# Performance work log

Hardware: AMD Instinct MI355X
Metric: run time of the kernel (lower is better)

Reference implementation:

```python
import math
import jax, jax.numpy as jnp
import numpy as np

B, L, HID = 2, 2048, 2048
H = 16
D = HID // H  # 128
EPS = 1e-6
ROPE_BASE = 10000.0
BETA_MIN, BETA_MAX = 0.8, 0.9995


def _rope_cache(seq_len, dim):
    half = dim // 2
    inv_freq = 1.0 / (ROPE_BASE ** (jnp.arange(half, dtype=jnp.float32) / float(half)))
    t = jnp.arange(seq_len, dtype=jnp.float32)
    freqs = t[:, None] * inv_freq[None, :]  # [L, half]
    return jnp.cos(freqs), jnp.sin(freqs)


def _apply_rope(x, cos, sin):
    # x: [B, H, L, D]; cos/sin: [L, D//2]
    half = x.shape[-1] // 2
    xe, xo = x[..., :half], x[..., half:]
    c = cos[None, None]
    s = sin[None, None]
    return jnp.concatenate([xe * c - xo * s, xe * s + xo * c], axis=-1)


def setup_inputs() -> dict:
    key = jax.random.key(0)
    ks = jax.random.split(key, 6)
    sc = 1.0 / math.sqrt(HID)  # ~ xavier scale
    return {
        "x": jax.random.normal(ks[0], (B, L, HID), jnp.float32),
        "Wq": jax.random.normal(ks[1], (HID, HID), jnp.float32) * sc,
        "Wk": jax.random.normal(ks[2], (HID, HID), jnp.float32) * sc,
        "Wv": jax.random.normal(ks[3], (HID, HID), jnp.float32) * sc,
        "Wg": jax.random.normal(ks[4], (HID, H), jnp.float32) * sc,
        "bg": jnp.full((H,), math.log(0.98 / (1.0 - 0.98)), jnp.float32),
        "Wo": jax.random.normal(ks[5], (HID, HID), jnp.float32) * sc,
        "bo": jnp.zeros((HID,), jnp.float32),
    }


def _deltanet(x, Wq, Wk, Wv, Wg, bg, Wo, bo):
    Bb, Ll, _ = x.shape
    split = lambda t: t.reshape(Bb, Ll, H, D).transpose(0, 2, 1, 3)  # [B,H,L,D]
    q = split(x @ Wq)
    k = split(x @ Wk)
    v = split(x @ Wv)

    cos, sin = _rope_cache(Ll, D)
    q = _apply_rope(q, cos, sin)
    k = _apply_rope(k, cos, sin)

    beta = jax.nn.sigmoid(x @ Wg + bg)                # [B,L,H]
    beta = jnp.clip(beta, BETA_MIN, BETA_MAX).transpose(0, 2, 1)  # [B,H,L]

    phi_q = jax.nn.elu(q) + 1.0
    phi_k = jax.nn.elu(k) + 1.0

    # time-major for scan
    pq = phi_q.transpose(2, 0, 1, 3)  # [L,B,H,D]
    pk = phi_k.transpose(2, 0, 1, 3)
    vt = v.transpose(2, 0, 1, 3)
    bt = beta.transpose(2, 0, 1)      # [L,B,H]

    S0 = jnp.zeros((Bb, H, D, D), jnp.float32)
    z0 = jnp.zeros((Bb, H, D), jnp.float32)

    def step(carry, inp):
        S, z = carry
        pq_t, pk_t, v_t, b_t = inp
        S = S * b_t[..., None, None] + pk_t[..., :, None] * v_t[..., None, :]
        z = z * b_t[..., None] + pk_t
        numer = jnp.einsum('bhd,bhde->bhe', pq_t, S)
        denom = jnp.sum(pq_t * z, axis=-1, keepdims=True) + EPS
        return (S, z), numer / denom

    (_, _), y = jax.lax.scan(step, (S0, z0), (pq, pk, vt, bt))  # y: [L,B,H,D]
    y = y.transpose(1, 0, 2, 3).reshape(Bb, Ll, HID)  # [B,L,H*D]
    return y @ Wo + bo


def reference(x, Wq, Wk, Wv, Wg, bg, Wo, bo):
    return _deltanet(x, Wq, Wk, Wv, Wg, bg, Wo, bo)
```

## Files before the change

### kernel.cpp

```cpp
#include <hip/hip_runtime.h>


typedef __attribute__((ext_vector_type(8))) short short8;
typedef __attribute__((ext_vector_type(4))) float f32x4;

__device__ __forceinline__ unsigned short f2bf(float f) {
  unsigned u = __float_as_uint(f);
  u += 0x7fffu + ((u >> 16) & 1u);
  return (unsigned short)(u >> 16);
}
__device__ __forceinline__ float bf2f(unsigned short s) {
  return __uint_as_float(((unsigned)s) << 16);
}
__device__ __forceinline__ float phi_elu1(float x) {
  return x > 0.f ? x + 1.f : expf(x);
}
__device__ __forceinline__ void gl_lds16(const void* g, void* l) {
  __builtin_amdgcn_global_load_lds(
      (const __attribute__((address_space(1))) void*)g,
      (__attribute__((address_space(3))) void*)l, 16, 0, 0);
}
__device__ __forceinline__ void bar_raw() {
  asm volatile("" ::: "memory");
  __builtin_amdgcn_s_barrier();
  asm volatile("" ::: "memory");
}

__global__ __launch_bounds__(256)
void k_cast(const float* __restrict__ x, unsigned short* __restrict__ xb) {
  int i = (blockIdx.x * 256 + threadIdx.x) * 4;
  float4 f = *(const float4*)(x + i);
  uint2 p;
  p.x = (unsigned)f2bf(f.x) | ((unsigned)f2bf(f.y) << 16);
  p.y = (unsigned)f2bf(f.z) | ((unsigned)f2bf(f.w) << 16);
  *(uint2*)(xb + i) = p;
}

__global__ __launch_bounds__(256)
void k_transw(const float* __restrict__ Wq, const float* __restrict__ Wk,
              const float* __restrict__ Wv, const float* __restrict__ Wo,
              const float* __restrict__ Wg,
              unsigned short* __restrict__ Wt, unsigned short* __restrict__ Wot,
              unsigned short* __restrict__ Wgt16) {
  const int z = blockIdx.z;
  if (z == 4) {
    if (blockIdx.y != 0) return;
    int idx = blockIdx.x * 256 + threadIdx.x;
    int h = idx >> 9, k4 = (idx & 511) * 4;
    uint2 p;
    p.x = (unsigned)f2bf(Wg[(k4 + 0) * 16 + h]) | ((unsigned)f2bf(Wg[(k4 + 1) * 16 + h]) << 16);
    p.y = (unsigned)f2bf(Wg[(k4 + 2) * 16 + h]) | ((unsigned)f2bf(Wg[(k4 + 3) * 16 + h]) << 16);
    *(uint2*)(Wgt16 + (size_t)h * 2048 + k4) = p;
    return;
  }
  const float* W = (z == 0) ? Wq : (z == 1) ? Wk : (z == 2) ? Wv : Wo;
  unsigned short* out = (z < 3) ? (Wt + (size_t)z * 2048 * 2048) : Wot;
  __shared__ float tile[64][65];
  const int n0 = blockIdx.x * 64;
  const int k0 = blockIdx.y * 64;
  const int tx = threadIdx.x & 63;
  const int ty = threadIdx.x >> 6;
#pragma unroll
  for (int rl = 0; rl < 16; ++rl) {
    int kk = rl * 4 + ty;
    tile[kk][tx] = W[(size_t)(k0 + kk) * 2048 + n0 + tx];
  }
  __syncthreads();
#pragma unroll
  for (int rl = 0; rl < 16; ++rl) {
    int nn = rl * 4 + ty;
    out[(size_t)(n0 + nn) * 2048 + k0 + tx] = f2bf(tile[tx][nn]);
  }
}

__global__ __launch_bounds__(256)
void k_betaW(const unsigned short* __restrict__ xb, const unsigned short* __restrict__ Wgt16,
             const float* __restrict__ bg, float* __restrict__ beta) {
  const int w = threadIdx.x >> 6;
  const int lane = threadIdx.x & 63;
  const int m = blockIdx.x * 4 + w;
  const int h = lane & 15, kq = lane >> 4;
  const unsigned short* xr = xb + (size_t)m * 2048 + kq * 512;
  const unsigned short* wr = Wgt16 + (size_t)h * 2048 + kq * 512;
  float acc = 0.f;
#pragma unroll 8
  for (int i = 0; i < 64; ++i) {
    short8 xv = *(const short8*)(xr + i * 8);
    short8 wv = *(const short8*)(wr + i * 8);
#pragma unroll
    for (int j = 0; j < 8; ++j)
      acc = fmaf(bf2f((unsigned short)xv[j]), bf2f((unsigned short)wv[j]), acc);
  }
  acc += __shfl_xor(acc, 16, 64);
  acc += __shfl_xor(acc, 32, 64);
  if (lane < 16) {
    float v = acc + bg[h];
    float bv = 1.f / (1.f + expf(-v));
    beta[(size_t)m * 16 + h] = fminf(fmaxf(bv, 0.8f), 0.9995f);
  }
}

template <bool OUT_BF16, bool ADD_BIAS>
__global__ __launch_bounds__(512, 2)
void k_gemm2(const unsigned short* __restrict__ A, const unsigned short* __restrict__ Bt,
             void* __restrict__ Cptr, const float* __restrict__ bias,
             int M, int N, int K, int ldA, int ldC) {
  __shared__ __align__(16) unsigned short Ls[3][3][128][64];
  const int tid = threadIdx.x;
  const int lane = tid & 63;
  const int w = tid >> 6;
  const int wm = w >> 1;
  const int wn = w & 1;
  const int ql = lane >> 4;
  const int r = lane & 15;

  const int nwg = gridDim.x * gridDim.y;
  const int orig = blockIdx.y * gridDim.x + blockIdx.x;
  const int li = (orig & 7) * (nwg >> 3) + (orig >> 3);
  const int m0 = (li & 15) * 256;
  const int n0 = (li >> 4) * 128;

  const int srow = tid >> 3;
  const int sphys = tid & 7;
  const int slog = sphys ^ (srow & 7);
  const unsigned short* Ab = A + (size_t)(m0 + srow) * ldA + slog * 8;
  const unsigned short* Bb = Bt + (size_t)(n0 + srow) * K + slog * 8;

#define STG(st, h, tt)                                                        \
  do {                                                                        \
    const size_t ldx = ((h) == 2) ? (size_t)K : (size_t)ldA;                  \
    const unsigned short* gs =                                                \
        (((h) == 2) ? Bb : (Ab + (size_t)((h) * 128) * ldA)) +                \
        (size_t)(tt) * 64;                                                    \
    unsigned short* ld = &Ls[(st)][(h)][srow][sphys * 8];                     \
    gl_lds16(gs, ld);                                                         \
    gl_lds16(gs + 64 * ldx, ld + 64 * 64);                                    \
  } while (0)

  f32x4 acc[4][4];
#pragma unroll
  for (int i = 0; i < 4; ++i)
#pragma unroll
    for (int j = 0; j < 4; ++j) acc[i][j] = (f32x4){0.f, 0.f, 0.f, 0.f};

  const int NT = K >> 6;

#pragma unroll
  for (int h = 0; h < 3; ++h) STG(0, h, 0);
#pragma unroll
  for (int h = 0; h < 3; ++h) STG(1, h, 1);
  asm volatile("s_waitcnt vmcnt(6)" ::: "memory");
  bar_raw();

  short8 bfr[4][2];

  for (int t = 0; t < NT; ++t) {
    const int st = t % 3;
    const unsigned short (*LA)[64] = Ls[st][wm >> 1];
    const unsigned short (*LB)[64] = Ls[st][2];
    const int arow0 = (wm & 1) * 64;
    const int brow0 = wn * 64;
    const bool pf = (t + 2 < NT);
    const int s2 = (t + 2) % 3;
#pragma unroll
    for (int p = 0; p < 2; ++p) {
      if (p == 0) {
#pragma unroll
        for (int nj = 0; nj < 4; ++nj)
#pragma unroll
          for (int kk = 0; kk < 2; ++kk)
            bfr[nj][kk] = *(const short8*)
                &LB[brow0 + nj * 16 + r][((kk * 4 + ql) ^ (r & 7)) * 8];
      }
      short8 af[2][2];
#pragma unroll
      for (int im = 0; im < 2; ++im)
#pragma unroll
        for (int kk = 0; kk < 2; ++kk)
          af[im][kk] = *(const short8*)
              &LA[arow0 + (p * 2 + im) * 16 + r][((kk * 4 + ql) ^ (r & 7)) * 8];
      if (pf) {
        if (p == 0) {
          STG(s2, 0, t + 2);
          STG(s2, 1, t + 2);
        } else {
          STG(s2, 2, t + 2);
        }
      }
      bar_raw();
      asm volatile("s_waitcnt lgkmcnt(0)" ::: "memory");
      __builtin_amdgcn_sched_barrier(0);
      __builtin_amdgcn_s_setprio(1);
#pragma unroll
      for (int kk = 0; kk < 2; ++kk)
#pragma unroll
        for (int im = 0; im < 2; ++im)
#pragma unroll
          for (int nj = 0; nj < 4; ++nj)
            acc[p * 2 + im][nj] = __builtin_amdgcn_mfma_f32_16x16x32_bf16(
                af[im][kk], bfr[nj][kk], acc[p * 2 + im][nj], 0, 0, 0);
      __builtin_amdgcn_s_setprio(0);
      if (p == 1) {
        if (pf)
          asm volatile("s_waitcnt vmcnt(6)" ::: "memory");
        else if (t + 1 < NT)
          asm volatile("s_waitcnt vmcnt(0)" ::: "memory");
      }
      bar_raw();
    }
  }
#undef STG

#pragma unroll
  for (int mi = 0; mi < 4; ++mi) {
#pragma unroll
    for (int nj = 0; nj < 4; ++nj) {
#pragma unroll
      for (int rr = 0; rr < 4; ++rr) {
        int mrow = m0 + wm * 64 + mi * 16 + ql * 4 + rr;
        int ncol = n0 + wn * 64 + nj * 16 + r;
        float val = acc[mi][nj][rr];
        if (ADD_BIAS) val += bias[ncol];
        if (OUT_BF16)
          ((unsigned short*)Cptr)[(size_t)mrow * ldC + ncol] = f2bf(val);
        else
          ((float*)Cptr)[(size_t)mrow * ldC + ncol] = val;
      }
    }
  }
}

__global__ __launch_bounds__(256)
void k_prep(const unsigned short* __restrict__ qkv, const float* __restrict__ beta,
            unsigned short* __restrict__ Qt, unsigned short* __restrict__ Ktg,
            unsigned short* __restrict__ Ag, float* __restrict__ gch) {
  const int ch = blockIdx.x;
  const int bh = blockIdx.y;
  const int b = bh >> 4, h = bh & 15;
  const int tid = threadIdx.x;
  const int t0 = ch * 64;

  __shared__ float Gs[64];
  __shared__ unsigned short Qs[64][136];
  __shared__ unsigned short Ks[64][136];

  if (tid < 64) {
    float bb = beta[((size_t)(b * 2048 + t0 + tid)) * 16 + h];
#pragma unroll
    for (int off = 1; off < 64; off <<= 1) {
      float o = __shfl_up(bb, off, 64);
      if (tid >= off) bb *= o;
    }
    Gs[tid] = bb;
    if (tid == 63) gch[bh * 32 + ch] = bb;
  }
  __syncthreads();

  const int dgl = tid & 7;
  float invf[8];
#pragma unroll
  for (int j = 0; j < 8; ++j)
    invf[j] = expf((float)(dgl * 8 + j) * -0.14391156831212787f);

  int s = tid >> 3;
#pragma unroll
  for (int rep = 0; rep < 2; ++rep, s += 32) {
    size_t row = ((size_t)(b * 2048 + t0 + s)) * 6144 + (size_t)h * 128;
    short8 qlo = *(const short8*)(qkv + row + dgl * 8);
    short8 qhi = *(const short8*)(qkv + row + 64 + dgl * 8);
    short8 klo = *(const short8*)(qkv + row + 2048 + dgl * 8);
    short8 khi = *(const short8*)(qkv + row + 2048 + 64 + dgl * 8);
    float g = Gs[s];
    float ig = 1.f / g;
    float tg = (float)(t0 + s);
    short8 oql, oqh, okl, okh;
#pragma unroll
    for (int j = 0; j < 8; ++j) {
      float sn, cs;
      __sincosf(tg * invf[j], &sn, &cs);
      float qe = bf2f((unsigned short)qlo[j]), qo = bf2f((unsigned short)qhi[j]);
      float a0 = qe * cs - qo * sn, a1 = qe * sn + qo * cs;
      oql[j] = (short)f2bf(phi_elu1(a0) * g);
      oqh[j] = (short)f2bf(phi_elu1(a1) * g);
      float ke = bf2f((unsigned short)klo[j]), ko = bf2f((unsigned short)khi[j]);
      a0 = ke * cs - ko * sn;
      a1 = ke * sn + ko * cs;
      okl[j] = (short)f2bf(phi_elu1(a0) * ig);
      okh[j] = (short)f2bf(phi_elu1(a1) * ig);
    }
    size_t qbase = (((size_t)bh * 32 + ch) * 64 + s) * 128;
    *(short8*)(Qt + qbase + dgl * 8) = oql;
    *(short8*)(Qt + qbase + 64 + dgl * 8) = oqh;
    *(short8*)&Qs[s][dgl * 8] = oql;
    *(short8*)&Qs[s][64 + dgl * 8] = oqh;
    *(short8*)&Ks[s][dgl * 8] = okl;
    *(short8*)&Ks[s][64 + dgl * 8] = okh;
  }
  __syncthreads();

  {
    const int d = tid >> 1, sh = tid & 1;
    unsigned pk[16];
#pragma unroll
    for (int i = 0; i < 16; ++i)
      pk[i] = (unsigned)Ks[sh * 32 + 2 * i][d] | ((unsigned)Ks[sh * 32 + 2 * i + 1][d] << 16);
    unsigned short* kr = Ktg + ((size_t)bh * 32 + ch) * 8192 + (size_t)d * 64 + sh * 32;
#pragma unroll
    for (int i = 0; i < 4; ++i)
      *(uint4*)(kr + i * 8) = *(uint4*)&pk[i * 4];
  }

  {
    const int lane = tid & 63;
    const int w = tid >> 6;
    const int q = lane >> 4, r = lane & 15;
    f32x4 acc[4];
#pragma unroll
    for (int nt = 0; nt < 4; ++nt) acc[nt] = (f32x4){0.f, 0.f, 0.f, 0.f};
#pragma unroll
    for (int kk = 0; kk < 4; ++kk) {
      short8 af = *(const short8*)&Qs[w * 16 + r][kk * 32 + q * 8];
#pragma unroll
      for (int nt = 0; nt < 4; ++nt) {
        short8 bf = *(const short8*)&Ks[nt * 16 + r][kk * 32 + q * 8];
        acc[nt] = __builtin_amdgcn_mfma_f32_16x16x32_bf16(af, bf, acc[nt], 0, 0, 0);
      }
    }
    unsigned short* Agp = Ag + ((size_t)bh * 32 + ch) * 4096;
#pragma unroll
    for (int nt = 0; nt < 4; ++nt) {
#pragma unroll
      for (int rr = 0; rr < 4; ++rr) {
        int t_l = w * 16 + q * 4 + rr;
        int s_l = nt * 16 + r;
        float val = (s_l <= t_l) ? acc[nt][rr] : 0.f;
        Agp[t_l * 64 + s_l] = f2bf(val);
      }
    }
  }
}

__global__ __launch_bounds__(256)
void k_scan(const unsigned short* __restrict__ Qt, const unsigned short* __restrict__ Ktg,
            const unsigned short* __restrict__ Ag, const unsigned short* __restrict__ qkv,
            const float* __restrict__ gch, unsigned short* __restrict__ numerb) {
  const int eb = blockIdx.x;
  const int bh = blockIdx.y;
  const int b = bh >> 4, h = bh & 15;
  const int tid = threadIdx.x;
  const int lane = tid & 63;
  const int w = tid >> 6;
  const int q = lane >> 4, r = lane & 15;
  const int e0 = eb * 16;

  __shared__ unsigned short Qs[64][136];
  __shared__ unsigned short Kts[128][72];
  __shared__ unsigned short As[64][72];
  __shared__ unsigned short Vt[16][72];
  __shared__ unsigned short SbT[16][136];
  __shared__ __align__(16) float zbuf[2][128];

  f32x4 S_acc[2];
  S_acc[0] = (f32x4){0.f, 0.f, 0.f, 0.f};
  S_acc[1] = (f32x4){0.f, 0.f, 0.f, 0.f};
  if (tid < 128) zbuf[0][tid] = 0.f;

  for (int ch = 0; ch < 32; ++ch) {
    const int cur = ch & 1, nxt = cur ^ 1;
    __syncthreads();
    {
      const unsigned short* Qg = Qt + ((size_t)bh * 32 + ch) * 8192;
#pragma unroll
      for (int i = 0; i < 4; ++i) {
        int c = tid + i * 256;
        int ss = c >> 4, dg = c & 15;
        *(int4*)&Qs[ss][dg * 8] = *(const int4*)(Qg + ss * 128 + dg * 8);
      }
      const unsigned short* Kg = Ktg + ((size_t)bh * 32 + ch) * 8192;
#pragma unroll
      for (int i = 0; i < 4; ++i) {
        int c = tid + i * 256;
        int d = c >> 3, sg = c & 7;
        *(int4*)&Kts[d][sg * 8] = *(const int4*)(Kg + d * 64 + sg * 8);
      }
      const unsigned short* Agp = Ag + ((size_t)bh * 32 + ch) * 4096;
#pragma unroll
      for (int i = 0; i < 2; ++i) {
        int c = tid + i * 256;
        int t_l = c >> 3, sg = c & 7;
        *(int4*)&As[t_l][sg * 8] = *(const int4*)(Agp + t_l * 64 + sg * 8);
      }
      {
        int ss = tid >> 2, e4 = tid & 3;
        const unsigned short* vp =
            qkv + ((size_t)(b * 2048 + ch * 64 + ss)) * 6144 + 4096 + h * 128 + e0 + e4 * 4;
        uint2 vv = *(const uint2*)vp;
        const unsigned short* pv = (const unsigned short*)&vv;
#pragma unroll
        for (int j = 0; j < 4; ++j) Vt[e4 * 4 + j][ss] = pv[j];
      }
#pragma unroll
      for (int i = 0; i < 2; ++i)
#pragma unroll
        for (int rr = 0; rr < 4; ++rr)
          SbT[r][(2 * w + i) * 16 + q * 4 + rr] = f2bf(S_acc[i][rr]);
    }
    __syncthreads();

    const float gc = gch[bh * 32 + ch];

    f32x4 nacc = (f32x4){0.f, 0.f, 0.f, 0.f};
    float dsum = 0.f;
#pragma unroll
    for (int kk = 0; kk < 4; ++kk) {
      short8 af = *(const short8*)&Qs[w * 16 + r][kk * 32 + q * 8];
      short8 bf = *(const short8*)&SbT[r][kk * 32 + q * 8];
      nacc = __builtin_amdgcn_mfma_f32_16x16x32_bf16(af, bf, nacc, 0, 0, 0);
      const float* zp = &zbuf[cur][kk * 32 + q * 8];
      float4 z0a = *(const float4*)zp;
      float4 z0b = *(const float4*)(zp + 4);
      dsum = fmaf(bf2f((unsigned short)af[0]), z0a.x, dsum);
      dsum = fmaf(bf2f((unsigned short)af[1]), z0a.y, dsum);
      dsum = fmaf(bf2f((unsigned short)af[2]), z0a.z, dsum);
      dsum = fmaf(bf2f((unsigned short)af[3]), z0a.w, dsum);
      dsum = fmaf(bf2f((unsigned short)af[4]), z0b.x, dsum);
      dsum = fmaf(bf2f((unsigned short)af[5]), z0b.y, dsum);
      dsum = fmaf(bf2f((unsigned short)af[6]), z0b.z, dsum);
      dsum = fmaf(bf2f((unsigned short)af[7]), z0b.w, dsum);
    }
    short8 vf[2];
#pragma unroll
    for (int kk = 0; kk < 2; ++kk) {
      vf[kk] = *(const short8*)&Vt[r][kk * 32 + q * 8];
      short8 af = *(const short8*)&As[w * 16 + r][kk * 32 + q * 8];
      nacc = __builtin_amdgcn_mfma_f32_16x16x32_bf16(af, vf[kk], nacc, 0, 0, 0);
#pragma unroll
      for (int j = 0; j < 8; ++j) dsum += bf2f((unsigned short)af[j]);
    }
    dsum += __shfl_xor(dsum, 16, 64);
    dsum += __shfl_xor(dsum, 32, 64);
    float inv = 1.f / (dsum + 1e-6f);
#pragma unroll
    for (int rr = 0; rr < 4; ++rr) {
      float inv_r = __shfl(inv, q * 4 + rr, 64);
      int t_l = w * 16 + q * 4 + rr;
      size_t m = (size_t)b * 2048 + ch * 64 + t_l;
      numerb[m * 2048 + h * 128 + e0 + r] = f2bf(nacc[rr] * inv_r);
    }

    {
      int d = tid >> 1, half = tid & 1;
      const unsigned short* kp = &Kts[d][half * 32];
      float zs = 0.f;
#pragma unroll
      for (int i = 0; i < 4; ++i) {
        short8 kv = *(const short8*)(kp + i * 8);
#pragma unroll
        for (int j = 0; j < 8; ++j) zs += bf2f((unsigned short)kv[j]);
      }
      zs += __shfl_xor(zs, 1, 64);
      if (half == 0) zbuf[nxt][d] = gc * (zbuf[cur][d] + zs);
    }

#pragma unroll
    for (int i = 0; i < 2; ++i) {
#pragma unroll
      for (int kk = 0; kk < 2; ++kk) {
        short8 af = *(const short8*)&Kts[(2 * w + i) * 16 + r][kk * 32 + q * 8];
        S_acc[i] = __builtin_amdgcn_mfma_f32_16x16x32_bf16(af, vf[kk], S_acc[i], 0, 0, 0);
      }
#pragma unroll
      for (int rr = 0; rr < 4; ++rr) S_acc[i][rr] *= gc;
    }
  }
}

extern "C" void kernel_launch(void* const* d_in, const int* in_sizes, int n_in,
                              void* d_out, int out_size, void* d_ws, size_t ws_size,
                              hipStream_t stream) {
  const float* x  = (const float*)d_in[0];
  const float* Wq = (const float*)d_in[1];
  const float* Wk = (const float*)d_in[2];
  const float* Wv = (const float*)d_in[3];
  const float* Wg = (const float*)d_in[4];
  const float* bg = (const float*)d_in[5];
  const float* Wo = (const float*)d_in[6];
  const float* bo = (const float*)d_in[7];

  char* ws = (char*)d_ws;
  unsigned short* xb    = (unsigned short*)(ws);
  unsigned short* Qt    = (unsigned short*)(ws);
  unsigned short* Wt    = (unsigned short*)(ws + 16777216);
  unsigned short* Ktg   = (unsigned short*)(ws + 16777216);
  unsigned short* Ag    = (unsigned short*)(ws + 33554432);
  unsigned short* Wot   = (unsigned short*)(ws + 41943040);
  unsigned short* qkvb  = (unsigned short*)(ws + 50331648);
  float*          beta  = (float*)(ws + 100663296);
  unsigned short* Wgt16 = (unsigned short*)(ws + 101187584);
  unsigned short* numerb= (unsigned short*)(ws + 101187584);
  float*          gch   = (float*)d_out;

  k_cast<<<8192, 256, 0, stream>>>(x, xb);
  k_transw<<<dim3(32, 32, 5), 256, 0, stream>>>(Wq, Wk, Wv, Wo, Wg, Wt, Wot, Wgt16);
  k_gemm2<true, false><<<dim3(16, 48), 512, 0, stream>>>(
      xb, Wt, qkvb, nullptr, 4096, 6144, 2048, 2048, 6144);
  k_betaW<<<1024, 256, 0, stream>>>(xb, Wgt16, bg, beta);
  k_prep<<<dim3(32, 32), 256, 0, stream>>>(qkvb, beta, Qt, Ktg, Ag, gch);
  k_scan<<<dim3(8, 32), 256, 0, stream>>>(Qt, Ktg, Ag, qkvb, gch, numerb);
  k_gemm2<false, true><<<dim3(16, 16), 512, 0, stream>>>(
      numerb, Wot, d_out, bo, 4096, 2048, 2048, 2048, 2048);
}
```

Baseline: 426.6 us.

## Replace QKV GEMM with simple kernel, restructure scan per head, tweak gemm2 scheduling

```diff
diff --git a/kernel.cpp b/kernel.cpp
--- a/kernel.cpp
+++ b/kernel.cpp
@@ -101,6 +101,81 @@
 }
 
 template <bool OUT_BF16, bool ADD_BIAS>
+__global__ __launch_bounds__(256)
+void k_gemm(const unsigned short* __restrict__ A, const unsigned short* __restrict__ Bt,
+            void* __restrict__ Cptr, const float* __restrict__ bias,
+            int M, int N, int K, int ldA, int ldC) {
+  __shared__ __align__(16) unsigned short As[128][64];
+  __shared__ __align__(16) unsigned short Bs[128][64];
+  const int tid = threadIdx.x;
+  const int n0 = blockIdx.x * 128;
+  const int m0 = blockIdx.y * 128;
+  const int lane = tid & 63;
+  const int w = tid >> 6;
+  const int wm = w >> 1, wn = w & 1;
+  const int q = lane >> 4, r = lane & 15;
+
+  const int srow0 = w * 8 + (lane >> 3);
+  const int scol = ((lane & 7) ^ ((lane >> 3) & 7)) * 8;
+
+  f32x4 acc[4][4];
+#pragma unroll
+  for (int i = 0; i < 4; ++i)
+#pragma unroll
+    for (int j = 0; j < 4; ++j) acc[i][j] = (f32x4){0.f, 0.f, 0.f, 0.f};
+
+  const unsigned short* A0 = A + (size_t)(m0 + srow0) * ldA + scol;
+  const unsigned short* B0 = Bt + (size_t)(n0 + srow0) * K + scol;
+  unsigned short* lA = &As[srow0][(lane & 7) * 8];
+  unsigned short* lB = &Bs[srow0][(lane & 7) * 8];
+
+  const int rsw = r & 7;
+
+  for (int kt = 0; kt < K; kt += 64) {
+    __syncthreads();
+#pragma unroll
+    for (int i = 0; i < 4; ++i) {
+      gl_lds16(A0 + (size_t)i * 32 * ldA + kt, lA + i * 2048);
+      gl_lds16(B0 + (size_t)i * 32 * K + kt, lB + i * 2048);
+    }
+    __syncthreads();
+#pragma unroll
+    for (int kk = 0; kk < 2; ++kk) {
+      const int ps = ((kk * 4 + q) ^ rsw) * 8;
+      short8 af[4], bfr[4];
+#pragma unroll
+      for (int i = 0; i < 4; ++i)
+        af[i] = *(const short8*)&As[wm * 64 + i * 16 + r][ps];
+#pragma unroll
+      for (int j = 0; j < 4; ++j)
+        bfr[j] = *(const short8*)&Bs[wn * 64 + j * 16 + r][ps];
+#pragma unroll
+      for (int i = 0; i < 4; ++i)
+#pragma unroll
+        for (int j = 0; j < 4; ++j)
+          acc[i][j] = __builtin_amdgcn_mfma_f32_16x16x32_bf16(af[i], bfr[j], acc[i][j], 0, 0, 0);
+    }
+  }
+#pragma unroll
+  for (int i = 0; i < 4; ++i) {
+#pragma unroll
+    for (int j = 0; j < 4; ++j) {
+#pragma unroll
+      for (int rr = 0; rr < 4; ++rr) {
+        int mi = m0 + wm * 64 + i * 16 + q * 4 + rr;
+        int ni = n0 + wn * 64 + j * 16 + r;
+        float val = acc[i][j][rr];
+        if (ADD_BIAS) val += bias[ni];
+        if (OUT_BF16)
+          ((unsigned short*)Cptr)[(size_t)mi * ldC + ni] = f2bf(val);
+        else
+          ((float*)Cptr)[(size_t)mi * ldC + ni] = val;
+      }
+    }
+  }
+}
+
+template <bool OUT_BF16, bool ADD_BIAS>
 __global__ __launch_bounds__(512, 2)
 void k_gemm2(const unsigned short* __restrict__ A, const unsigned short* __restrict__ Bt,
              void* __restrict__ Cptr, const float* __restrict__ bias,
@@ -188,8 +263,6 @@
         }
       }
       bar_raw();
-      asm volatile("s_waitcnt lgkmcnt(0)" ::: "memory");
-      __builtin_amdgcn_sched_barrier(0);
       __builtin_amdgcn_s_setprio(1);
 #pragma unroll
       for (int kk = 0; kk < 2; ++kk)
@@ -206,6 +279,7 @@
         else if (t + 1 < NT)
           asm volatile("s_waitcnt vmcnt(0)" ::: "memory");
       }
+      __builtin_amdgcn_sched_barrier(0);
       bar_raw();
     }
   }
@@ -340,29 +414,28 @@
   }
 }
 
-__global__ __launch_bounds__(256)
+__global__ __launch_bounds__(512)
 void k_scan(const unsigned short* __restrict__ Qt, const unsigned short* __restrict__ Ktg,
             const unsigned short* __restrict__ Ag, const unsigned short* __restrict__ qkv,
             const float* __restrict__ gch, unsigned short* __restrict__ numerb) {
-  const int eb = blockIdx.x;
-  const int bh = blockIdx.y;
+  const int bh = blockIdx.x;
   const int b = bh >> 4, h = bh & 15;
   const int tid = threadIdx.x;
   const int lane = tid & 63;
   const int w = tid >> 6;
   const int q = lane >> 4, r = lane & 15;
-  const int e0 = eb * 16;
 
   __shared__ unsigned short Qs[64][136];
   __shared__ unsigned short Kts[128][72];
   __shared__ unsigned short As[64][72];
-  __shared__ unsigned short Vt[16][72];
-  __shared__ unsigned short SbT[16][136];
+  __shared__ unsigned short Vt[128][72];
+  __shared__ unsigned short SbT[8][16][136];
   __shared__ __align__(16) float zbuf[2][128];
-
-  f32x4 S_acc[2];
-  S_acc[0] = (f32x4){0.f, 0.f, 0.f, 0.f};
-  S_acc[1] = (f32x4){0.f, 0.f, 0.f, 0.f};
+  __shared__ float invs[64];
+
+  f32x4 S_acc[8];
+#pragma unroll
+  for (int i = 0; i < 8; ++i) S_acc[i] = (f32x4){0.f, 0.f, 0.f, 0.f};
   if (tid < 128) zbuf[0][tid] = 0.f;
 
   for (int ch = 0; ch < 32; ++ch) {
@@ -371,106 +444,136 @@
     {
       const unsigned short* Qg = Qt + ((size_t)bh * 32 + ch) * 8192;
 #pragma unroll
-      for (int i = 0; i < 4; ++i) {
-        int c = tid + i * 256;
+      for (int i = 0; i < 2; ++i) {
+        int c = tid + i * 512;
         int ss = c >> 4, dg = c & 15;
         *(int4*)&Qs[ss][dg * 8] = *(const int4*)(Qg + ss * 128 + dg * 8);
       }
       const unsigned short* Kg = Ktg + ((size_t)bh * 32 + ch) * 8192;
 #pragma unroll
-      for (int i = 0; i < 4; ++i) {
-        int c = tid + i * 256;
+      for (int i = 0; i < 2; ++i) {
+        int c = tid + i * 512;
         int d = c >> 3, sg = c & 7;
         *(int4*)&Kts[d][sg * 8] = *(const int4*)(Kg + d * 64 + sg * 8);
       }
       const unsigned short* Agp = Ag + ((size_t)bh * 32 + ch) * 4096;
+      {
+        int t_l = tid >> 3, sg = tid & 7;
+        *(int4*)&As[t_l][sg * 8] = *(const int4*)(Agp + t_l * 64 + sg * 8);
+      }
+      {
+        int ss = tid >> 3, ef = tid & 7;
+        const unsigned short* vrow =
+            qkv + ((size_t)(b * 2048 + ch * 64 + ss)) * 6144 + 4096 + h * 128;
+#pragma unroll
+        for (int rep = 0; rep < 4; ++rep) {
+          int e4 = ef + rep * 8;
+          uint2 vv = *(const uint2*)(vrow + e4 * 4);
+          const unsigned short* pv = (const unsigned short*)&vv;
+#pragma unroll
+          for (int j = 0; j < 4; ++j) Vt[e4 * 4 + j][ss] = pv[j];
+        }
+      }
+#pragma unroll
+      for (int ib = 0; ib < 8; ++ib) {
+        uint2 pk;
+        pk.x = (unsigned)f2bf(S_acc[ib][0]) | ((unsigned)f2bf(S_acc[ib][1]) << 16);
+        pk.y = (unsigned)f2bf(S_acc[ib][2]) | ((unsigned)f2bf(S_acc[ib][3]) << 16);
+        *(uint2*)&SbT[w][r][ib * 16 + q * 4] = pk;
+      }
+    }
+    __syncthreads();
+
+    const float gc = gch[bh * 32 + ch];
+
+    f32x4 nacc[4];
+#pragma unroll
+    for (int wb = 0; wb < 4; ++wb) nacc[wb] = (f32x4){0.f, 0.f, 0.f, 0.f};
+#pragma unroll
+    for (int kk = 0; kk < 4; ++kk) {
+      short8 sb = *(const short8*)&SbT[w][r][kk * 32 + q * 8];
+#pragma unroll
+      for (int wb = 0; wb < 4; ++wb) {
+        short8 aq = *(const short8*)&Qs[wb * 16 + r][kk * 32 + q * 8];
+        nacc[wb] = __builtin_amdgcn_mfma_f32_16x16x32_bf16(aq, sb, nacc[wb], 0, 0, 0);
+      }
+    }
+    short8 vf[2];
+#pragma unroll
+    for (int kk = 0; kk < 2; ++kk) {
+      vf[kk] = *(const short8*)&Vt[w * 16 + r][kk * 32 + q * 8];
+#pragma unroll
+      for (int wb = 0; wb < 4; ++wb) {
+        short8 aa = *(const short8*)&As[wb * 16 + r][kk * 32 + q * 8];
+        nacc[wb] = __builtin_amdgcn_mfma_f32_16x16x32_bf16(aa, vf[kk], nacc[wb], 0, 0, 0);
+      }
+    }
+
+    if (w < 4) {
+      float dsum = 0.f;
+#pragma unroll
+      for (int kk = 0; kk < 4; ++kk) {
+        short8 aq = *(const short8*)&Qs[w * 16 + r][kk * 32 + q * 8];
+        const float* zp = &zbuf[cur][kk * 32 + q * 8];
+        float4 z0a = *(const float4*)zp;
+        float4 z0b = *(const float4*)(zp + 4);
+        dsum = fmaf(bf2f((unsigned short)aq[0]), z0a.x, dsum);
+        dsum = fmaf(bf2f((unsigned short)aq[1]), z0a.y, dsum);
+        dsum = fmaf(bf2f((unsigned short)aq[2]), z0a.z, dsum);
+        dsum = fmaf(bf2f((unsigned short)aq[3]), z0a.w, dsum);
+        dsum = fmaf(bf2f((unsigned short)aq[4]), z0b.x, dsum);
+        dsum = fmaf(bf2f((unsigned short)aq[5]), z0b.y, dsum);
+        dsum = fmaf(bf2f((unsigned short)aq[6]), z0b.z, dsum);
+        dsum = fmaf(bf2f((unsigned short)aq[7]), z0b.w, dsum);
+      }
+#pragma unroll
+      for (int kk = 0; kk < 2; ++kk) {
+        short8 aa = *(const short8*)&As[w * 16 + r][kk * 32 + q * 8];
+#pragma unroll
+        for (int j = 0; j < 8; ++j) dsum += bf2f((unsigned short)aa[j]);
+      }
+      dsum += __shfl_xor(dsum, 16, 64);
+      dsum += __shfl_xor(dsum, 32, 64);
+      if (lane < 16) invs[w * 16 + lane] = 1.f / (dsum + 1e-6f);
+    }
+
+    {
+      int d = tid >> 2, qt = tid & 3;
+      const unsigned short* kp = &Kts[d][qt * 16];
+      float zs = 0.f;
 #pragma unroll
       for (int i = 0; i < 2; ++i) {
-        int c = tid + i * 256;
-        int t_l = c >> 3, sg = c & 7;
-        *(int4*)&As[t_l][sg * 8] = *(const int4*)(Agp + t_l * 64 + sg * 8);
-      }
-      {
-        int ss = tid >> 2, e4 = tid & 3;
-        const unsigned short* vp =
-            qkv + ((size_t)(b * 2048 + ch * 64 + ss)) * 6144 + 4096 + h * 128 + e0 + e4 * 4;
-        uint2 vv = *(const uint2*)vp;
-        const unsigned short* pv = (const unsigned short*)&vv;
-#pragma unroll
-        for (int j = 0; j < 4; ++j) Vt[e4 * 4 + j][ss] = pv[j];
-      }
-#pragma unroll
-      for (int i = 0; i < 2; ++i)
-#pragma unroll
-        for (int rr = 0; rr < 4; ++rr)
-          SbT[r][(2 * w + i) * 16 + q * 4 + rr] = f2bf(S_acc[i][rr]);
-    }
+        short8 kv = *(const short8*)(kp + i * 8);
+#pragma unroll
+        for (int j = 0; j < 8; ++j) zs += bf2f((unsigned short)kv[j]);
+      }
+      zs += __shfl_xor(zs, 1, 64);
+      zs += __shfl_xor(zs, 2, 64);
+      if (qt == 0) zbuf[nxt][d] = gc * (zbuf[cur][d] + zs);
+    }
+
+#pragma unroll
+    for (int ib = 0; ib < 8; ++ib) {
+#pragma unroll
+      for (int kk = 0; kk < 2; ++kk) {
+        short8 ak = *(const short8*)&Kts[ib * 16 + r][kk * 32 + q * 8];
+        S_acc[ib] = __builtin_amdgcn_mfma_f32_16x16x32_bf16(ak, vf[kk], S_acc[ib], 0, 0, 0);
+      }
+#pragma unroll
+      for (int rr = 0; rr < 4; ++rr) S_acc[ib][rr] *= gc;
+    }
+
     __syncthreads();
 
-    const float gc = gch[bh * 32 + ch];
-
-    f32x4 nacc = (f32x4){0.f, 0.f, 0.f, 0.f};
-    float dsum = 0.f;
-#pragma unroll
-    for (int kk = 0; kk < 4; ++kk) {
-      short8 af = *(const short8*)&Qs[w * 16 + r][kk * 32 + q * 8];
-      short8 bf = *(const short8*)&SbT[r][kk * 32 + q * 8];
-      nacc = __builtin_amdgcn_mfma_f32_16x16x32_bf16(af, bf, nacc, 0, 0, 0);
-      const float* zp = &zbuf[cur][kk * 32 + q * 8];
-      float4 z0a = *(const float4*)zp;
-      float4 z0b = *(const float4*)(zp + 4);
-      dsum = fmaf(bf2f((unsigned short)af[0]), z0a.x, dsum);
-      dsum = fmaf(bf2f((unsigned short)af[1]), z0a.y, dsum);
-      dsum = fmaf(bf2f((unsigned short)af[2]), z0a.z, dsum);
-      dsum = fmaf(bf2f((unsigned short)af[3]), z0a.w, dsum);
-      dsum = fmaf(bf2f((unsigned short)af[4]), z0b.x, dsum);
-      dsum = fmaf(bf2f((unsigned short)af[5]), z0b.y, dsum);
-      dsum = fmaf(bf2f((unsigned short)af[6]), z0b.z, dsum);
-      dsum = fmaf(bf2f((unsigned short)af[7]), z0b.w, dsum);
-    }
-    short8 vf[2];
-#pragma unroll
-    for (int kk = 0; kk < 2; ++kk) {
-      vf[kk] = *(const short8*)&Vt[r][kk * 32 + q * 8];
-      short8 af = *(const short8*)&As[w * 16 + r][kk * 32 + q * 8];
-      nacc = __builtin_amdgcn_mfma_f32_16x16x32_bf16(af, vf[kk], nacc, 0, 0, 0);
-#pragma unroll
-      for (int j = 0; j < 8; ++j) dsum += bf2f((unsigned short)af[j]);
-    }
-    dsum += __shfl_xor(dsum, 16, 64);
-    dsum += __shfl_xor(dsum, 32, 64);
-    float inv = 1.f / (dsum + 1e-6f);
-#pragma unroll
-    for (int rr = 0; rr < 4; ++rr) {
-      float inv_r = __shfl(inv, q * 4 + rr, 64);
-      int t_l = w * 16 + q * 4 + rr;
-      size_t m = (size_t)b * 2048 + ch * 64 + t_l;
-      numerb[m * 2048 + h * 128 + e0 + r] = f2bf(nacc[rr] * inv_r);
-    }
-
-    {
-      int d = tid >> 1, half = tid & 1;
-      const unsigned short* kp = &Kts[d][half * 32];
-      float zs = 0.f;
-#pragma unroll
-      for (int i = 0; i < 4; ++i) {
-        short8 kv = *(const short8*)(kp + i * 8);
-#pragma unroll
-        for (int j = 0; j < 8; ++j) zs += bf2f((unsigned short)kv[j]);
-      }
-      zs += __shfl_xor(zs, 1, 64);
-      if (half == 0) zbuf[nxt][d] = gc * (zbuf[cur][d] + zs);
-    }
-
-#pragma unroll
-    for (int i = 0; i < 2; ++i) {
-#pragma unroll
-      for (int kk = 0; kk < 2; ++kk) {
-        short8 af = *(const short8*)&Kts[(2 * w + i) * 16 + r][kk * 32 + q * 8];
-        S_acc[i] = __builtin_amdgcn_mfma_f32_16x16x32_bf16(af, vf[kk], S_acc[i], 0, 0, 0);
-      }
-#pragma unroll
-      for (int rr = 0; rr < 4; ++rr) S_acc[i][rr] *= gc;
+#pragma unroll
+    for (int wb = 0; wb < 4; ++wb) {
+#pragma unroll
+      for (int rr = 0; rr < 4; ++rr) {
+        int t_l = wb * 16 + q * 4 + rr;
+        float inv_r = invs[t_l];
+        size_t m = (size_t)b * 2048 + ch * 64 + t_l;
+        numerb[m * 2048 + h * 128 + w * 16 + r] = f2bf(nacc[wb][rr] * inv_r);
+      }
     }
   }
 }
@@ -502,11 +605,11 @@
 
   k_cast<<<8192, 256, 0, stream>>>(x, xb);
   k_transw<<<dim3(32, 32, 5), 256, 0, stream>>>(Wq, Wk, Wv, Wo, Wg, Wt, Wot, Wgt16);
-  k_gemm2<true, false><<<dim3(16, 48), 512, 0, stream>>>(
+  k_gemm<true, false><<<dim3(48, 32), 256, 0, stream>>>(
       xb, Wt, qkvb, nullptr, 4096, 6144, 2048, 2048, 6144);
   k_betaW<<<1024, 256, 0, stream>>>(xb, Wgt16, bg, beta);
   k_prep<<<dim3(32, 32), 256, 0, stream>>>(qkvb, beta, Qt, Ktg, Ag, gch);
-  k_scan<<<dim3(8, 32), 256, 0, stream>>>(Qt, Ktg, Ag, qkvb, gch, numerb);
+  k_scan<<<32, 512, 0, stream>>>(Qt, Ktg, Ag, qkvb, gch, numerb);
   k_gemm2<false, true><<<dim3(16, 16), 512, 0, stream>>>(
       numerb, Wot, d_out, bo, 4096, 2048, 2048, 2048, 2048);
 }
```

Result: slower. 469.8 us (+10.1%).
